# Performance work log

Measured on AMD Instinct MI355X. Metric: run time of the kernel, lower is better.

## Reference

```python
import jax, jax.numpy as jnp
import numpy as np

C, B, F, O, DK = 10, 8192, 256, 64, 5


def setup_inputs() -> dict:
    key = jax.random.key(0)
    ks = jax.random.split(key, 7)
    x = jax.random.normal(ks[0], (B, F), jnp.float32)
    y = jax.random.normal(ks[1], (B, C), jnp.float32)
    # kaiming-uniform-like init scales
    w_key = jax.random.normal(ks[2], (C, 1, 1, DK), jnp.float32) * 0.5
    w_query = jax.random.normal(ks[3], (C, 1, DK), jnp.float32) * 0.5
    w_value = jax.random.normal(ks[4], (C, 1, 1), jnp.float32) * 0.5
    weight = jax.random.normal(ks[5], (C, 1, F, O), jnp.float32) * (1.0 / np.sqrt(F))
    bias = jax.random.normal(ks[6], (C, 1, O), jnp.float32) * 0.1
    return {"x": x, "y": y, "w_key": w_key, "w_query": w_query,
            "w_value": w_value, "weight": weight, "bias": bias}


def reference(x, y, w_key, w_query, w_value, weight, bias):
    # x: [B,F] (first=True -> conceptually [1,B,F]); y: [B,C]
    yt = y.T                                             # [C,B]
    querys = yt[..., None] * w_query                     # [C,B,1]*[C,1,DK] -> [C,B,DK]
    # keys[c,b,f,k] = x[b,f] * w_key[c,k]; attn_scores[c,b,f] = sum_k keys*querys
    #              = x[b,f] * (w_key[c] . querys[c,b])  (rank-1 structure, fused)
    kq = jnp.einsum('ck,cbk->cb', w_key.reshape(w_key.shape[0], -1), querys)  # [C,B]
    # mean over batch dim, then softmax over features
    scores_avg = jnp.einsum('bf,cb->cf', x, kq) / x.shape[0]  # [C,F]
    sm = jax.nn.softmax(scores_avg, axis=-1)                  # [C,F]
    attn = sm / jnp.max(sm, axis=-1, keepdims=True)           # [C,F] max-normalized
    values = x[None, :, :] * w_value                          # [1,B,F]*[C,1,1] -> [C,B,F]
    weighted = values * attn[:, None, :]                      # [C,B,F]
    # (weighted[...,None,:] @ weight).squeeze() + bias -> [C,B,O]
    out = jnp.einsum('cbf,cfo->cbo', weighted, weight[:, 0]) + bias  # bias [C,1,O]
    return out
```

## Files before the change

kernel.cpp:

```cpp
#include <hip/hip_runtime.h>
#include <hip/hip_bf16.h>

#define C_ 10
#define B_ 8192
#define F_ 256
#define O_ 64
#define DK_ 5

typedef __attribute__((ext_vector_type(8))) short short8;
typedef __attribute__((ext_vector_type(4))) float floatx4;

static __device__ __forceinline__ unsigned short f2bf(float f) {
    union { float f; unsigned u; } v; v.f = f;
    unsigned r = v.u + 0x7fffu + ((v.u >> 16) & 1u);
    return (unsigned short)(r >> 16);
}

__global__ __launch_bounds__(256) void k1_reduce(const float* __restrict__ x,
                                                 const float* __restrict__ y,
                                                 float* __restrict__ G,
                                                 unsigned short* __restrict__ xb) {
    __shared__ float xl[32 * F_];
    __shared__ float yl[32 * C_];
    const int b0 = blockIdx.x * 32;
    const int t  = threadIdx.x;

    for (int i = t; i < 32 * C_; i += 256) yl[i] = y[b0 * C_ + i];

    const int r  = t >> 6;
    const int f4 = (t & 63) * 4;
#pragma unroll
    for (int j = 0; j < 8; ++j) {
        int row = r + 4 * j;
        float4 v = *(const float4*)(x + (size_t)(b0 + row) * F_ + f4);
        *(float4*)(xl + row * F_ + f4) = v;
        ushort4 s;
        s.x = f2bf(v.x); s.y = f2bf(v.y); s.z = f2bf(v.z); s.w = f2bf(v.w);
        *(ushort4*)(xb + (size_t)(b0 + row) * F_ + f4) = s;
    }
    __syncthreads();

    float acc[C_];
#pragma unroll
    for (int c = 0; c < C_; ++c) acc[c] = 0.f;

#pragma unroll 8
    for (int b = 0; b < 32; ++b) {
        float xv = xl[b * F_ + t];
#pragma unroll
        for (int c = 0; c < C_; ++c) acc[c] = fmaf(yl[b * C_ + c], xv, acc[c]);
    }
#pragma unroll
    for (int c = 0; c < C_; ++c) atomicAdd(&G[c * F_ + t], acc[c]);
}

__global__ __launch_bounds__(256) void k2_wprep(const float* __restrict__ G,
                                                const float* __restrict__ w_key,
                                                const float* __restrict__ w_query,
                                                const float* __restrict__ w_value,
                                                const float* __restrict__ weight,
                                                unsigned short* __restrict__ WT) {
    __shared__ float a2[F_];
    __shared__ float wred[4];
    const int c    = blockIdx.x >> 2;
    const int part = blockIdx.x & 3;
    const int t    = threadIdx.x;

    float s = 0.f;
#pragma unroll
    for (int k = 0; k < DK_; ++k) s += w_key[c * DK_ + k] * w_query[c * DK_ + k];

    float z = s * G[c * F_ + t] * (1.0f / (float)B_);
    float m = z;
#pragma unroll
    for (int off = 32; off >= 1; off >>= 1) m = fmaxf(m, __shfl_xor(m, off));
    if ((t & 63) == 0) wred[t >> 6] = m;
    __syncthreads();
    float mm = fmaxf(fmaxf(wred[0], wred[1]), fmaxf(wred[2], wred[3]));
    a2[t] = expf(z - mm) * w_value[c];
    __syncthreads();

    const int o  = t & 63;
    const int fg = t >> 6;
    const float* wsrc = weight + (size_t)c * F_ * O_;
    char* wdst = (char*)(WT + (size_t)c * O_ * F_);
#pragma unroll
    for (int g = 0; g < 2; ++g) {
        int f0 = part * 64 + fg * 16 + g * 8;
        short8 v8;
#pragma unroll
        for (int e = 0; e < 8; ++e) {
            int f = f0 + e;
            v8[e] = (short)f2bf(wsrc[f * O_ + o] * a2[f]);
        }
        int byte = o * 512 + ((2 * f0) ^ ((o & 7) << 4));
        *(short8*)(wdst + byte) = v8;
    }
}

__global__ __launch_bounds__(256) void k3_mfma(const unsigned short* __restrict__ xb,
                                               const unsigned short* __restrict__ WT,
                                               const float* __restrict__ bias,
                                               float* __restrict__ out) {
    __shared__ unsigned short wt[O_ * F_];
    const int c  = blockIdx.y;
    const int b0 = blockIdx.x * 64;
    const int t  = threadIdx.x;
    const int w  = t >> 6;
    const int l  = t & 63;
    const int lr = l & 15;
    const int lg = l >> 4;

    const unsigned short* xrow = xb + (size_t)(b0 + w * 16 + lr) * F_;
    short8 a[8];
#pragma unroll
    for (int k0 = 0; k0 < 8; ++k0) a[k0] = *(const short8*)(xrow + k0 * 32 + lg * 8);

    {
        const short8* src = (const short8*)(WT + (size_t)c * O_ * F_);
        short8* dst = (short8*)wt;
#pragma unroll
        for (int j = 0; j < 8; ++j) dst[t + 256 * j] = src[t + 256 * j];
    }
    __syncthreads();

    floatx4 acc[4];
#pragma unroll
    for (int n = 0; n < 4; ++n) {
        float bo = bias[c * O_ + n * 16 + lr];
        acc[n] = (floatx4){bo, bo, bo, bo};
    }

#pragma unroll
    for (int k0 = 0; k0 < 8; ++k0) {
#pragma unroll
        for (int n = 0; n < 4; ++n) {
            int o = n * 16 + lr;
            int byte = o * 512 + ((k0 * 64 + lg * 16) ^ ((o & 7) << 4));
            short8 bf = *(const short8*)((const char*)wt + byte);
            acc[n] = __builtin_amdgcn_mfma_f32_16x16x32_bf16(a[k0], bf, acc[n], 0, 0, 0);
        }
    }

#pragma unroll
    for (int n = 0; n < 4; ++n) {
        int col = n * 16 + lr;
#pragma unroll
        for (int r = 0; r < 4; ++r) {
            int row = b0 + w * 16 + lg * 4 + r;
            out[((size_t)c * B_ + row) * O_ + col] = acc[n][r];
        }
    }
}

extern "C" void kernel_launch(void* const* d_in, const int* in_sizes, int n_in,
                              void* d_out, int out_size, void* d_ws, size_t ws_size,
                              hipStream_t stream) {
    const float* x       = (const float*)d_in[0];
    const float* y       = (const float*)d_in[1];
    const float* w_key   = (const float*)d_in[2];
    const float* w_query = (const float*)d_in[3];
    const float* w_value = (const float*)d_in[4];
    const float* weight  = (const float*)d_in[5];
    const float* bias    = (const float*)d_in[6];
    float* out = (float*)d_out;

    char* ws = (char*)d_ws;
    float*          G  = (float*)ws;
    unsigned short* xb = (unsigned short*)(ws + 16384);
    unsigned short* WT = (unsigned short*)(ws + 16384 + (size_t)B_ * F_ * 2);

    hipMemsetAsync(G, 0, C_ * F_ * sizeof(float), stream);
    k1_reduce<<<B_ / 32, 256, 0, stream>>>(x, y, G, xb);
    k2_wprep<<<C_ * 4, 256, 0, stream>>>(G, w_key, w_query, w_value, weight, WT);
    dim3 g3(B_ / 64, C_);
    k3_mfma<<<g3, 256, 0, stream>>>(xb, WT, bias, out);
}
```

Baseline: 34.45 us.

## Replace atomic accumulation with per-block partials reduced in weight-prep kernel

```diff
diff --git a/kernel.cpp b/kernel.cpp
--- a/kernel.cpp
+++ b/kernel.cpp
@@ -6,6 +6,7 @@
 #define F_ 256
 #define O_ 64
 #define DK_ 5
+#define NBLK1 256
 
 typedef __attribute__((ext_vector_type(8))) short short8;
 typedef __attribute__((ext_vector_type(4))) float floatx4;
@@ -18,7 +19,7 @@
 
 __global__ __launch_bounds__(256) void k1_reduce(const float* __restrict__ x,
                                                  const float* __restrict__ y,
-                                                 float* __restrict__ G,
+                                                 float* __restrict__ G_part,
                                                  unsigned short* __restrict__ xb) {
     __shared__ float xl[32 * F_];
     __shared__ float yl[32 * C_];
@@ -50,11 +51,13 @@
 #pragma unroll
         for (int c = 0; c < C_; ++c) acc[c] = fmaf(yl[b * C_ + c], xv, acc[c]);
     }
+
+    float* gp = G_part + (size_t)blockIdx.x * C_ * F_ + t;
 #pragma unroll
-    for (int c = 0; c < C_; ++c) atomicAdd(&G[c * F_ + t], acc[c]);
+    for (int c = 0; c < C_; ++c) gp[c * F_] = acc[c];
 }
 
-__global__ __launch_bounds__(256) void k2_wprep(const float* __restrict__ G,
+__global__ __launch_bounds__(256) void k2_wprep(const float* __restrict__ G_part,
                                                 const float* __restrict__ w_key,
                                                 const float* __restrict__ w_query,
                                                 const float* __restrict__ w_value,
@@ -66,11 +69,22 @@
     const int part = blockIdx.x & 3;
     const int t    = threadIdx.x;
 
+    const float* gp = G_part + c * F_ + t;
+    float g0 = 0.f, g1 = 0.f, g2 = 0.f, g3 = 0.f;
+#pragma unroll 4
+    for (int blk = 0; blk < NBLK1; blk += 4) {
+        g0 += gp[(size_t)(blk + 0) * C_ * F_];
+        g1 += gp[(size_t)(blk + 1) * C_ * F_];
+        g2 += gp[(size_t)(blk + 2) * C_ * F_];
+        g3 += gp[(size_t)(blk + 3) * C_ * F_];
+    }
+    float g = (g0 + g1) + (g2 + g3);
+
     float s = 0.f;
 #pragma unroll
     for (int k = 0; k < DK_; ++k) s += w_key[c * DK_ + k] * w_query[c * DK_ + k];
 
-    float z = s * G[c * F_ + t] * (1.0f / (float)B_);
+    float z = s * g * (1.0f / (float)B_);
     float m = z;
 #pragma unroll
     for (int off = 32; off >= 1; off >>= 1) m = fmaxf(m, __shfl_xor(m, off));
@@ -85,8 +99,8 @@
     const float* wsrc = weight + (size_t)c * F_ * O_;
     char* wdst = (char*)(WT + (size_t)c * O_ * F_);
 #pragma unroll
-    for (int g = 0; g < 2; ++g) {
-        int f0 = part * 64 + fg * 16 + g * 8;
+    for (int gi = 0; gi < 2; ++gi) {
+        int f0 = part * 64 + fg * 16 + gi * 8;
         short8 v8;
 #pragma unroll
         for (int e = 0; e < 8; ++e) {
@@ -166,13 +180,12 @@
     float* out = (float*)d_out;
 
     char* ws = (char*)d_ws;
-    float*          G  = (float*)ws;
-    unsigned short* xb = (unsigned short*)(ws + 16384);
-    unsigned short* WT = (unsigned short*)(ws + 16384 + (size_t)B_ * F_ * 2);
+    unsigned short* xb     = (unsigned short*)ws;
+    unsigned short* WT     = (unsigned short*)(ws + (size_t)B_ * F_ * 2);
+    float*          G_part = (float*)(ws + (size_t)B_ * F_ * 2 + C_ * O_ * F_ * 2);
 
-    hipMemsetAsync(G, 0, C_ * F_ * sizeof(float), stream);
-    k1_reduce<<<B_ / 32, 256, 0, stream>>>(x, y, G, xb);
-    k2_wprep<<<C_ * 4, 256, 0, stream>>>(G, w_key, w_query, w_value, weight, WT);
+    k1_reduce<<<NBLK1, 256, 0, stream>>>(x, y, G_part, xb);
+    k2_wprep<<<C_ * 4, 256, 0, stream>>>(G_part, w_key, w_query, w_value, weight, WT);
     dim3 g3(B_ / 64, C_);
     k3_mfma<<<g3, 256, 0, stream>>>(xb, WT, bias, out);
 }
```

New measurement: 40.96 us. 1.19x slower.
